# Kernel optimization log

Measured on AMD Instinct MI355X. Metric: run time of the kernel, lower is better.

Reference implementation:

```python
import jax, jax.numpy as jnp
import numpy as np

NUM_HEADS = 16
ROPE_BASE = 10000.0


def _rope_interleaved(x, cos, sin):
    # x: (B, S, H, hd); cos/sin: (1, S, 1, hd//2)
    x1 = x[..., ::2]
    x2 = x[..., 1::2]
    r1 = x1 * cos - x2 * sin
    r2 = x1 * sin + x2 * cos
    return jnp.stack([r1, r2], axis=-1).reshape(x.shape)


def _rope_tables(seq_len, head_dim, dtype):
    dim = head_dim // 2
    freqs = jnp.exp(-jnp.arange(0, dim, dtype=dtype) * jnp.log(jnp.asarray(ROPE_BASE, dtype)) / dim)
    pos = jnp.arange(seq_len, dtype=dtype)
    angles = pos[:, None] * freqs[None, :]  # (S, hd//2)
    return jnp.cos(angles)[None, :, None, :], jnp.sin(angles)[None, :, None, :]


def setup_inputs() -> dict:
    key = jax.random.key(0)
    ks = jax.random.split(key, 9)
    B, S, D = 2, 2048, 2048
    sc = 1.0 / np.sqrt(D)
    return {
        "x": jax.random.normal(ks[0], (B, S, D), jnp.float32),
        "wq": jax.random.normal(ks[1], (D, D), jnp.float32) * sc,
        "bq": jax.random.normal(ks[2], (D,), jnp.float32) * 0.01,
        "wk": jax.random.normal(ks[3], (D, D), jnp.float32) * sc,
        "bk": jax.random.normal(ks[4], (D,), jnp.float32) * 0.01,
        "wv": jax.random.normal(ks[5], (D, D), jnp.float32) * sc,
        "bv": jax.random.normal(ks[6], (D,), jnp.float32) * 0.01,
        "wo": jax.random.normal(ks[7], (D, D), jnp.float32) * sc,
        "bo": jax.random.normal(ks[8], (D,), jnp.float32) * 0.01,
    }


def reference(x, wq, bq, wk, bk, wv, bv, wo, bo):
    B, S, D = x.shape
    H = NUM_HEADS
    hd = D // H
    # QKV projections (eqx.nn.Linear: y = W @ x + b, weight (out, in))
    q = (x @ wq.T + bq).reshape(B, S, H, hd)
    k = (x @ wk.T + bk).reshape(B, S, H, hd)
    v = (x @ wv.T + bv).reshape(B, S, H, hd)
    # RoPE (interleaved / GPT-NeoX style)
    cos, sin = _rope_tables(S, hd, x.dtype)
    q = _rope_interleaved(q, cos, sin)
    k = _rope_interleaved(k, cos, sin)
    # Causal scaled dot-product attention
    scale = 1.0 / np.sqrt(hd)
    scores = jnp.einsum("bqhd,bkhd->bhqk", q, k) * scale
    causal = jnp.tril(jnp.ones((S, S), dtype=bool))
    scores = jnp.where(causal[None, None, :, :], scores, jnp.finfo(scores.dtype).min)
    attn = jax.nn.softmax(scores, axis=-1)
    out = jnp.einsum("bhqk,bkhd->bqhd", attn, v).reshape(B, S, D)
    return out @ wo.T + bo
```

## Files before the change

kernel.cpp:

```cpp
#include <hip/hip_runtime.h>

typedef unsigned short u16;
typedef short bf16x8 __attribute__((ext_vector_type(8)));
typedef float f32x4 __attribute__((ext_vector_type(4)));

#define B_ 2
#define S_ 2048
#define D_ 2048
#define HD_ 128
#define GW 512
#define KB 64
#define VST 72
#define PST 72

__device__ __forceinline__ float bf2f(u16 h) {
  unsigned u = ((unsigned)h) << 16;
  return __builtin_bit_cast(float, u);
}
__device__ __forceinline__ u16 f2bf(float f) {
  unsigned u = __builtin_bit_cast(unsigned, f);
  u += 0x7FFF + ((u >> 16) & 1);
  return (u16)(u >> 16);
}
__device__ __forceinline__ bf16x8 cvt8(const float* p) {
  float4 a = *(const float4*)p;
  float4 b = *(const float4*)(p + 4);
  bf16x8 r;
  r[0] = (short)f2bf(a.x); r[1] = (short)f2bf(a.y);
  r[2] = (short)f2bf(a.z); r[3] = (short)f2bf(a.w);
  r[4] = (short)f2bf(b.x); r[5] = (short)f2bf(b.y);
  r[6] = (short)f2bf(b.z); r[7] = (short)f2bf(b.w);
  return r;
}

__device__ __forceinline__ void gload16(const void* g, void* lds) {
  __builtin_amdgcn_global_load_lds(
      (const __attribute__((address_space(1))) unsigned*)g,
      (__attribute__((address_space(3))) unsigned*)lds, 16, 0, 0);
}

__device__ __forceinline__ f32x4 mfma16(bf16x8 a, bf16x8 b, f32x4 c) {
  return __builtin_amdgcn_mfma_f32_16x16x32_bf16(a, b, c, 0, 0, 0);
}

__global__ void k_cvt_all(const float* __restrict__ x, const float* __restrict__ wq,
                          const float* __restrict__ wk, const float* __restrict__ wv,
                          const float* __restrict__ wo, u16* __restrict__ xb,
                          u16* __restrict__ wqkvb, u16* __restrict__ wob) {
  const int slice = blockIdx.y;
  const int i = blockIdx.x * 256 + threadIdx.x;
  const float* src;
  u16* dst;
  int n8;
  if (slice == 0) { src = x; dst = xb; n8 = 1048576; }
  else if (slice == 1) { src = wq; dst = wqkvb; n8 = 524288; }
  else if (slice == 2) { src = wk; dst = wqkvb + 4194304; n8 = 524288; }
  else if (slice == 3) { src = wv; dst = wqkvb + 8388608; n8 = 524288; }
  else { src = wo; dst = wob; n8 = 524288; }
  if (i < n8) *(bf16x8*)(dst + (size_t)i * 8) = cvt8(src + (size_t)i * 8);
}

template <int AM, int WM, int CM>
__device__ __forceinline__ void gemm_body(const void* Ap, const void* Wp,
                                          const float* __restrict__ bias,
                                          void* Cp, int ldc) {
  constexpr int K = 2048;
  __shared__ u16 As[128 * 32];
  __shared__ u16 Bs[128 * 32];
  const int t = threadIdx.x;
  const int w = t >> 6, l = t & 63, lr = l & 15, lg = l >> 4;
  const int m0 = blockIdx.y * 128, n0 = blockIdx.x * 128;
  const int wr = w >> 1, wc = w & 1;

  f32x4 acc[4][4];
#pragma unroll
  for (int i = 0; i < 4; ++i)
#pragma unroll
    for (int j = 0; j < 4; ++j) acc[i][j] = f32x4{0.f, 0.f, 0.f, 0.f};

  const int rowA0 = t >> 2, ko0 = (t & 3) * 8;
  const int rowA1 = (t + 256) >> 2, ko1 = ((t + 256) & 3) * 8;

  for (int kt = 0; kt < K; kt += 32) {
    if constexpr (AM == 1) {
      const u16* A = (const u16*)Ap;
      gload16(A + (size_t)(m0 + rowA0) * K + kt + ko0, (char*)As + (size_t)w * 1024);
      gload16(A + (size_t)(m0 + rowA1) * K + kt + ko1, (char*)As + (size_t)(w + 4) * 1024);
    } else {
      const float* A = (const float*)Ap;
      *(bf16x8*)((char*)As + (size_t)t * 16) = cvt8(A + (size_t)(m0 + rowA0) * K + kt + ko0);
      *(bf16x8*)((char*)As + (size_t)(t + 256) * 16) = cvt8(A + (size_t)(m0 + rowA1) * K + kt + ko1);
    }
    if constexpr (WM == 1) {
      const u16* W = (const u16*)Wp;
      gload16(W + (size_t)(n0 + rowA0) * K + kt + ko0, (char*)Bs + (size_t)w * 1024);
      gload16(W + (size_t)(n0 + rowA1) * K + kt + ko1, (char*)Bs + (size_t)(w + 4) * 1024);
    } else {
      const float* W = (const float*)Wp;
      *(bf16x8*)((char*)Bs + (size_t)t * 16) = cvt8(W + (size_t)(n0 + rowA0) * K + kt + ko0);
      *(bf16x8*)((char*)Bs + (size_t)(t + 256) * 16) = cvt8(W + (size_t)(n0 + rowA1) * K + kt + ko1);
    }
    __syncthreads();

    bf16x8 af[4], bw[4];
#pragma unroll
    for (int i = 0; i < 4; ++i) {
      af[i] = *(const bf16x8*)(As + (size_t)(wr * 64 + i * 16 + lr) * 32 + lg * 8);
      bw[i] = *(const bf16x8*)(Bs + (size_t)(wc * 64 + i * 16 + lr) * 32 + lg * 8);
    }
#pragma unroll
    for (int i = 0; i < 4; ++i)
#pragma unroll
      for (int j = 0; j < 4; ++j)
        acc[i][j] = mfma16(af[i], bw[j], acc[i][j]);
    __syncthreads();
  }

#pragma unroll
  for (int i = 0; i < 4; ++i) {
#pragma unroll
    for (int j = 0; j < 4; ++j) {
      const int col = n0 + wc * 64 + j * 16 + lr;
      const float bv = bias[col];
      const int row = m0 + wr * 64 + i * 16 + lg * 4;
#pragma unroll
      for (int r = 0; r < 4; ++r) {
        if constexpr (CM == 1)
          ((float*)Cp)[(size_t)(row + r) * ldc + col] = acc[i][j][r] + bv;
        else
          ((u16*)Cp)[(size_t)(row + r) * ldc + col] = f2bf(acc[i][j][r] + bv);
      }
    }
  }
}

__global__ __launch_bounds__(256) void k_gemm_qkv_bb(
    const u16* __restrict__ xb, const u16* __restrict__ wqkvb,
    const float* __restrict__ bq, const float* __restrict__ bk,
    const float* __restrict__ bv, u16* __restrict__ q, u16* __restrict__ k,
    u16* __restrict__ v) {
  const int z = blockIdx.z;
  const u16* W = wqkvb + (size_t)z * D_ * D_;
  const float* bias = z == 0 ? bq : (z == 1 ? bk : bv);
  u16* C = z == 0 ? q : (z == 1 ? k : v);
  gemm_body<1, 1, 0>(xb, W, bias, C, D_);
}

__global__ __launch_bounds__(256) void k_gemm_out_bb(
    const u16* __restrict__ ao, const u16* __restrict__ wob,
    const float* __restrict__ bo, float* __restrict__ out) {
  gemm_body<1, 1, 1>(ao, wob, bo, out, D_);
}

__global__ __launch_bounds__(256) void k_gemm_qkv_xb(
    const u16* __restrict__ xb, const float* __restrict__ wq,
    const float* __restrict__ bq, const float* __restrict__ wk,
    const float* __restrict__ bk, const float* __restrict__ wv,
    const float* __restrict__ bv, u16* __restrict__ q, u16* __restrict__ k,
    u16* __restrict__ v) {
  const int z = blockIdx.z;
  const float* W = z == 0 ? wq : (z == 1 ? wk : wv);
  const float* bias = z == 0 ? bq : (z == 1 ? bk : bv);
  u16* C = z == 0 ? q : (z == 1 ? k : v);
  gemm_body<1, 0, 0>(xb, W, bias, C, D_);
}

__global__ __launch_bounds__(256) void k_gemm_out(const u16* __restrict__ ao,
                                                  const float* __restrict__ wo,
                                                  const float* __restrict__ bo,
                                                  float* __restrict__ out) {
  gemm_body<1, 0, 1>(ao, wo, bo, out, D_);
}

__global__ __launch_bounds__(256) void k_gemm_qkv_g(
    const float* __restrict__ x, const float* __restrict__ wq,
    const float* __restrict__ bq, const float* __restrict__ wk,
    const float* __restrict__ bk, const float* __restrict__ wv,
    const float* __restrict__ bv, u16* __restrict__ qg, u16* __restrict__ kg,
    u16* __restrict__ vg, int g) {
  const int z = blockIdx.z;
  const float* W = (z == 0 ? wq : (z == 1 ? wk : wv)) + (size_t)g * GW * D_;
  const float* bias = (z == 0 ? bq : (z == 1 ? bk : bv)) + g * GW;
  u16* C = z == 0 ? qg : (z == 1 ? kg : vg);
  gemm_body<0, 0, 0>(x, W, bias, C, GW);
}

__device__ __forceinline__ void rope_one(u16* p, float cv, float sv) {
  unsigned u = *(const unsigned*)p;
  float x1 = bf2f((u16)(u & 0xffff)), x2 = bf2f((u16)(u >> 16));
  unsigned r = (unsigned)f2bf(x1 * cv - x2 * sv) |
               ((unsigned)f2bf(x1 * sv + x2 * cv) << 16);
  *(unsigned*)p = r;
}

__global__ void k_rope_full(u16* q, u16* kk) {
  const int idx = blockIdx.x * 256 + threadIdx.x;
  const int i = idx & 63;
  const int hh = (idx >> 6) & 15;
  const int bs = idx >> 10;
  const int s = bs & (S_ - 1);
  const float freq = expf(-(float)i * 0.14391157f);
  float sv, cv;
  sincosf((float)s * freq, &sv, &cv);
  const size_t off = (size_t)bs * D_ + (size_t)hh * HD_ + 2 * i;
  rope_one(q + off, cv, sv);
  rope_one(kk + off, cv, sv);
}

__global__ void k_rope_g(u16* q, u16* kk) {
  const int idx = blockIdx.x * 256 + threadIdx.x;
  const int i = idx & 63;
  const int hh = (idx >> 6) & 3;
  const int bs = idx >> 8;
  const int s = bs & (S_ - 1);
  const float freq = expf(-(float)i * 0.14391157f);
  float sv, cv;
  sincosf((float)s * freq, &sv, &cv);
  const size_t off = (size_t)bs * GW + (size_t)hh * HD_ + 2 * i;
  rope_one(q + off, cv, sv);
  rope_one(kk + off, cv, sv);
}

__device__ __forceinline__ void attn_body(const u16* Q, const u16* Kd,
                                          const u16* V, u16* O,
                                          size_t base_in, size_t base_out,
                                          int ld_in, int ld_out, int q0) {
  const int t = threadIdx.x, w = t >> 6, l = t & 63, lr = l & 15, lg = l >> 4;

  __shared__ u16 Ks[KB * HD_];
  __shared__ u16 Vt[HD_ * VST];
  __shared__ u16 Ps[4][16 * PST];

  bf16x8 qf[4];
  {
    const u16* qp = Q + base_in + (size_t)(q0 + w * 16 + lr) * ld_in;
#pragma unroll
    for (int ds = 0; ds < 4; ++ds)
      qf[ds] = *(const bf16x8*)(qp + ds * 32 + lg * 8);
  }

  f32x4 oacc[8];
#pragma unroll
  for (int f = 0; f < 8; ++f) oacc[f] = f32x4{0.f, 0.f, 0.f, 0.f};
  float mrow = -1e30f, lrow = 0.f;

  const int qrow = q0 + w * 16 + lr;
  const int ntiles = q0 / KB + 1;
  const float sc = 0.08838834764831845f;

  for (int tkv = 0; tkv < ntiles; ++tkv) {
    const int kv0 = tkv * KB;
#pragma unroll
    for (int r = 0; r < 4; ++r) {
      const int c = t + 256 * r;
      const int row = c >> 4, c16 = c & 15;
      const int gc = c16 ^ (row & 7);
      gload16(Kd + base_in + (size_t)(kv0 + row) * ld_in + gc * 8,
              (char*)Ks + (size_t)(w + 4 * r) * 1024);
    }
#pragma unroll
    for (int r = 0; r < 2; ++r) {
      const int c = t + 256 * r;
      const int kk2 = (c & 31) * 2, d0 = (c >> 5) * 8;
      bf16x8 v0 = *(const bf16x8*)(V + base_in + (size_t)(kv0 + kk2) * ld_in + d0);
      bf16x8 v1 = *(const bf16x8*)(V + base_in + (size_t)(kv0 + kk2 + 1) * ld_in + d0);
#pragma unroll
      for (int j = 0; j < 8; ++j) {
        unsigned pk = (unsigned)(unsigned short)v0[j] |
                      ((unsigned)(unsigned short)v1[j] << 16);
        *(unsigned*)&Vt[(size_t)(d0 + j) * VST + kk2] = pk;
      }
    }
    __syncthreads();

    float p[16];
#pragma unroll
    for (int h = 0; h < 4; ++h) {
      f32x4 s = {0.f, 0.f, 0.f, 0.f};
#pragma unroll
      for (int ds = 0; ds < 4; ++ds) {
        const int ch = (ds * 4 + lg) ^ (lr & 7);
        bf16x8 kf = *(const bf16x8*)(Ks + (size_t)(h * 16 + lr) * HD_ + ch * 8);
        s = mfma16(kf, qf[ds], s);
      }
#pragma unroll
      for (int r = 0; r < 4; ++r) p[h * 4 + r] = s[r] * sc;
    }
    if (kv0 + KB - 1 > q0 + w * 16) {
#pragma unroll
      for (int h = 0; h < 4; ++h)
#pragma unroll
        for (int r = 0; r < 4; ++r)
          if (kv0 + h * 16 + lg * 4 + r > qrow) p[h * 4 + r] = -1e30f;
    }
    float pm = p[0];
#pragma unroll
    for (int i = 1; i < 16; ++i) pm = fmaxf(pm, p[i]);
    pm = fmaxf(pm, __shfl_xor(pm, 16, 64));
    pm = fmaxf(pm, __shfl_xor(pm, 32, 64));
    const float mn = fmaxf(mrow, pm);
    const float scl = __expf(mrow - mn);
    mrow = mn;
    float rs = 0.f;
#pragma unroll
    for (int i = 0; i < 16; ++i) {
      p[i] = __expf(p[i] - mn);
      rs += p[i];
    }
    rs += __shfl_xor(rs, 16, 64);
    rs += __shfl_xor(rs, 32, 64);
    lrow = lrow * scl + rs;
    float sj[4];
#pragma unroll
    for (int j = 0; j < 4; ++j) sj[j] = __shfl(scl, lg * 4 + j, 64);
#pragma unroll
    for (int f = 0; f < 8; ++f)
#pragma unroll
      for (int j = 0; j < 4; ++j) oacc[f][j] *= sj[j];
#pragma unroll
    for (int h = 0; h < 4; ++h)
#pragma unroll
      for (int r = 0; r < 4; ++r)
        Ps[w][lr * PST + h * 16 + lg * 4 + r] = f2bf(p[h * 4 + r]);
    bf16x8 pf0 = *(const bf16x8*)&Ps[w][lr * PST + lg * 8];
    bf16x8 pf1 = *(const bf16x8*)&Ps[w][lr * PST + 32 + lg * 8];
#pragma unroll
    for (int f = 0; f < 8; ++f) {
      bf16x8 vf0 = *(const bf16x8*)&Vt[(size_t)(f * 16 + lr) * VST + lg * 8];
      bf16x8 vf1 = *(const bf16x8*)&Vt[(size_t)(f * 16 + lr) * VST + 32 + lg * 8];
      oacc[f] = mfma16(pf0, vf0, oacc[f]);
      oacc[f] = mfma16(pf1, vf1, oacc[f]);
    }
    __syncthreads();
  }

  const float inv = 1.0f / lrow;
  float ij[4];
#pragma unroll
  for (int j = 0; j < 4; ++j) ij[j] = __shfl(inv, lg * 4 + j, 64);
  u16* Op = O + base_out;
#pragma unroll
  for (int f = 0; f < 8; ++f)
#pragma unroll
    for (int j = 0; j < 4; ++j)
      Op[(size_t)(q0 + w * 16 + lg * 4 + j) * ld_out + f * 16 + lr] =
          f2bf(oacc[f][j] * ij[j]);
}

__global__ __launch_bounds__(256) void k_attn_full(const u16* Q, const u16* Kd,
                                                   const u16* V, u16* O) {
  const int lin = blockIdx.y * gridDim.x + blockIdx.x;
  const int work = (lin & 7) * 64 + (lin >> 3);
  const int bh = work >> 4;
  const int pr = work & 15;
  const int b = bh >> 4, h = bh & 15;
  const size_t base = ((size_t)b * S_) * D_ + (size_t)h * HD_;
  attn_body(Q, Kd, V, O, base, base, D_, D_, 64 * (31 - pr));
  attn_body(Q, Kd, V, O, base, base, D_, D_, 64 * pr);
}

__global__ __launch_bounds__(256) void k_attn_g(const u16* __restrict__ Q,
                                                const u16* __restrict__ Kd,
                                                const u16* __restrict__ V,
                                                u16* __restrict__ O, int g) {
  const int by = blockIdx.y;
  const int b = by >> 2, hh = by & 3;
  const size_t base_in = ((size_t)b * S_) * GW + (size_t)hh * HD_;
  const size_t base_out = ((size_t)b * S_) * D_ + (size_t)(g * 4 + hh) * HD_;
  attn_body(Q, Kd, V, O, base_in, base_out, GW, D_, blockIdx.x * 64);
}

extern "C" void kernel_launch(void* const* d_in, const int* in_sizes, int n_in,
                              void* d_out, int out_size, void* d_ws,
                              size_t ws_size, hipStream_t stream) {
  (void)in_sizes; (void)n_in; (void)out_size;
  const float* x = (const float*)d_in[0];
  const float* wq = (const float*)d_in[1];
  const float* bq = (const float*)d_in[2];
  const float* wk = (const float*)d_in[3];
  const float* bk = (const float*)d_in[4];
  const float* wv = (const float*)d_in[5];
  const float* bv = (const float*)d_in[6];
  const float* wo = (const float*)d_in[7];
  const float* bo = (const float*)d_in[8];
  float* out = (float*)d_out;

  const size_t XB = (size_t)B_ * S_ * D_ * 2;
  const size_t WB3 = 3 * (size_t)D_ * D_ * 2;
  const size_t WB1 = (size_t)D_ * D_ * 2;
  char* ws = (char*)d_ws;
  char* ob = (char*)d_out;

  u16 *xb, *q, *k, *v, *wqkvb = nullptr, *wob = nullptr;
  int tier;
  if (ws_size >= 4 * XB + WB3 + WB1) {
    xb = (u16*)ws; q = (u16*)(ws + XB); k = (u16*)(ws + 2 * XB);
    v = (u16*)(ws + 3 * XB);
    wqkvb = (u16*)(ws + 4 * XB); wob = (u16*)(ws + 4 * XB + WB3);
    tier = 1;
  } else if (ws_size >= 3 * XB + WB3 + WB1) {
    xb = (u16*)ob;
    q = (u16*)ws; k = (u16*)(ws + XB); v = (u16*)(ws + 2 * XB);
    wqkvb = (u16*)(ws + 3 * XB); wob = (u16*)(ws + 3 * XB + WB3);
    tier = 1;
  } else if (ws_size >= 2 * XB + WB3 + WB1) {
    xb = (u16*)ob; v = (u16*)(ob + XB);
    q = (u16*)ws; k = (u16*)(ws + XB);
    wqkvb = (u16*)(ws + 2 * XB); wob = (u16*)(ws + 2 * XB + WB3);
    tier = 1;
  } else if (ws_size >= 2 * XB) {
    xb = (u16*)ob; v = (u16*)(ob + XB);
    q = (u16*)ws; k = (u16*)(ws + XB);
    tier = 2;
  } else {
    tier = 3;
  }

  if (tier == 1) {
    dim3 gc(4096, 5);
    k_cvt_all<<<gc, 256, 0, stream>>>(x, wq, wk, wv, wo, xb, wqkvb, wob);
    dim3 g1(16, 32, 3);
    k_gemm_qkv_bb<<<g1, 256, 0, stream>>>(xb, wqkvb, bq, bk, bv, q, k, v);
    k_rope_full<<<16384, 256, 0, stream>>>(q, k);
    dim3 g2(16, 32);
    k_attn_full<<<g2, 256, 0, stream>>>(q, k, v, q);
    dim3 g3(16, 32);
    k_gemm_out_bb<<<g3, 256, 0, stream>>>(q, wob, bo, out);
  } else if (tier == 2) {
    dim3 gc(4096, 1);
    k_cvt_all<<<gc, 256, 0, stream>>>(x, wq, wk, wv, wo, xb, xb, xb);
    dim3 g1(16, 32, 3);
    k_gemm_qkv_xb<<<g1, 256, 0, stream>>>(xb, wq, bq, wk, bk, wv, bv, q, k, v);
    k_rope_full<<<16384, 256, 0, stream>>>(q, k);
    dim3 g2(16, 32);
    k_attn_full<<<g2, 256, 0, stream>>>(q, k, v, q);
    dim3 g3(16, 32);
    k_gemm_out<<<g3, 256, 0, stream>>>(q, wo, bo, out);
  } else {
    u16* qg = (u16*)ob;
    u16* kg = qg + (size_t)(B_ * S_) * GW;
    u16* vg = kg + (size_t)(B_ * S_) * GW;
    u16* ao = (u16*)ws;
    for (int g = 0; g < 4; ++g) {
      dim3 g1(4, 32, 3);
      k_gemm_qkv_g<<<g1, 256, 0, stream>>>(x, wq, bq, wk, bk, wv, bv, qg, kg, vg, g);
      k_rope_g<<<4096, 256, 0, stream>>>(qg, kg);
      dim3 g2(32, 8);
      k_attn_g<<<g2, 256, 0, stream>>>(qg, kg, vg, ao, g);
    }
    dim3 g3(16, 32);
    k_gemm_out<<<g3, 256, 0, stream>>>(ao, wo, bo, out);
  }
}
```

Before: 293.0 us.

## Fuse RoPE into QKV GEMM epilogue and double-buffer K/V in attention

Precomputes a cos/sin table inside the conversion kernel and applies RoPE in the QKV GEMM epilogue, using a lane shuffle to pair interleaved columns. This removes the separate RoPE pass over Q and K. The attention loop now double-buffers K (async LDS loads) and V (register prefetch), uses explicit waitcnt/s_barrier and raises wave priority around the MFMA sections, so the next tile's loads overlap compute. Doubling the K/V shared memory may lower occupancy, and workspace tiers are reshuffled to hold the table.

```diff
diff --git a/kernel.cpp b/kernel.cpp
--- a/kernel.cpp
+++ b/kernel.cpp
@@ -46,9 +46,20 @@
 __global__ void k_cvt_all(const float* __restrict__ x, const float* __restrict__ wq,
                           const float* __restrict__ wk, const float* __restrict__ wv,
                           const float* __restrict__ wo, u16* __restrict__ xb,
-                          u16* __restrict__ wqkvb, u16* __restrict__ wob) {
+                          u16* __restrict__ wqkvb, u16* wob, float2* tab) {
   const int slice = blockIdx.y;
   const int i = blockIdx.x * 256 + threadIdx.x;
+  if (slice == 5) {
+    if (tab != nullptr && i < 131072) {
+      const int s = i >> 6, ip = i & 63;
+      const float freq = expf(-(float)ip * 0.14391157f);
+      float sv, cv;
+      sincosf((float)s * freq, &sv, &cv);
+      tab[i] = make_float2(cv, sv);
+    }
+    return;
+  }
+  if (slice == 4 && wob == nullptr) return;
   const float* src;
   u16* dst;
   int n8;
@@ -63,7 +74,8 @@
 template <int AM, int WM, int CM>
 __device__ __forceinline__ void gemm_body(const void* Ap, const void* Wp,
                                           const float* __restrict__ bias,
-                                          void* Cp, int ldc) {
+                                          void* Cp, int ldc,
+                                          const float2* __restrict__ tab) {
   constexpr int K = 2048;
   __shared__ u16 As[128 * 32];
   __shared__ u16 Bs[128 * 32];
@@ -123,12 +135,25 @@
       const int col = n0 + wc * 64 + j * 16 + lr;
       const float bv = bias[col];
       const int row = m0 + wr * 64 + i * 16 + lg * 4;
-#pragma unroll
-      for (int r = 0; r < 4; ++r) {
-        if constexpr (CM == 1)
-          ((float*)Cp)[(size_t)(row + r) * ldc + col] = acc[i][j][r] + bv;
-        else
-          ((u16*)Cp)[(size_t)(row + r) * ldc + col] = f2bf(acc[i][j][r] + bv);
+      if (CM == 0 && tab != nullptr) {
+        const int ip = (col & 127) >> 1;
+        const int odd = col & 1;
+#pragma unroll
+        for (int r = 0; r < 4; ++r) {
+          const float v = acc[i][j][r] + bv;
+          const float p = __shfl_xor(v, 1, 64);
+          const float2 cs = tab[((row + r) & (S_ - 1)) * 64 + ip];
+          const float o = odd ? (p * cs.y + v * cs.x) : (v * cs.x - p * cs.y);
+          ((u16*)Cp)[(size_t)(row + r) * ldc + col] = f2bf(o);
+        }
+      } else {
+#pragma unroll
+        for (int r = 0; r < 4; ++r) {
+          if constexpr (CM == 1)
+            ((float*)Cp)[(size_t)(row + r) * ldc + col] = acc[i][j][r] + bv;
+          else
+            ((u16*)Cp)[(size_t)(row + r) * ldc + col] = f2bf(acc[i][j][r] + bv);
+        }
       }
     }
   }
@@ -138,18 +163,18 @@
     const u16* __restrict__ xb, const u16* __restrict__ wqkvb,
     const float* __restrict__ bq, const float* __restrict__ bk,
     const float* __restrict__ bv, u16* __restrict__ q, u16* __restrict__ k,
-    u16* __restrict__ v) {
+    u16* __restrict__ v, const float2* __restrict__ tab) {
   const int z = blockIdx.z;
   const u16* W = wqkvb + (size_t)z * D_ * D_;
   const float* bias = z == 0 ? bq : (z == 1 ? bk : bv);
   u16* C = z == 0 ? q : (z == 1 ? k : v);
-  gemm_body<1, 1, 0>(xb, W, bias, C, D_);
+  gemm_body<1, 1, 0>(xb, W, bias, C, D_, z == 2 ? nullptr : tab);
 }
 
 __global__ __launch_bounds__(256) void k_gemm_out_bb(
     const u16* __restrict__ ao, const u16* __restrict__ wob,
     const float* __restrict__ bo, float* __restrict__ out) {
-  gemm_body<1, 1, 1>(ao, wob, bo, out, D_);
+  gemm_body<1, 1, 1>(ao, wob, bo, out, D_, nullptr);
 }
 
 __global__ __launch_bounds__(256) void k_gemm_qkv_xb(
@@ -162,14 +187,14 @@
   const float* W = z == 0 ? wq : (z == 1 ? wk : wv);
   const float* bias = z == 0 ? bq : (z == 1 ? bk : bv);
   u16* C = z == 0 ? q : (z == 1 ? k : v);
-  gemm_body<1, 0, 0>(xb, W, bias, C, D_);
+  gemm_body<1, 0, 0>(xb, W, bias, C, D_, nullptr);
 }
 
 __global__ __launch_bounds__(256) void k_gemm_out(const u16* __restrict__ ao,
                                                   const float* __restrict__ wo,
                                                   const float* __restrict__ bo,
                                                   float* __restrict__ out) {
-  gemm_body<1, 0, 1>(ao, wo, bo, out, D_);
+  gemm_body<1, 0, 1>(ao, wo, bo, out, D_, nullptr);
 }
 
 __global__ __launch_bounds__(256) void k_gemm_qkv_g(
@@ -182,7 +207,7 @@
   const float* W = (z == 0 ? wq : (z == 1 ? wk : wv)) + (size_t)g * GW * D_;
   const float* bias = (z == 0 ? bq : (z == 1 ? bk : bv)) + g * GW;
   u16* C = z == 0 ? qg : (z == 1 ? kg : vg);
-  gemm_body<0, 0, 0>(x, W, bias, C, GW);
+  gemm_body<0, 0, 0>(x, W, bias, C, GW, nullptr);
 }
 
 __device__ __forceinline__ void rope_one(u16* p, float cv, float sv) {
@@ -227,8 +252,8 @@
                                           int ld_in, int ld_out, int q0) {
   const int t = threadIdx.x, w = t >> 6, l = t & 63, lr = l & 15, lg = l >> 4;
 
-  __shared__ u16 Ks[KB * HD_];
-  __shared__ u16 Vt[HD_ * VST];
+  __shared__ u16 Ks[2][KB * HD_];
+  __shared__ u16 Vt[2][HD_ * VST];
   __shared__ u16 Ps[4][16 * PST];
 
   bf16x8 qf[4];
@@ -245,47 +270,90 @@
   float mrow = -1e30f, lrow = 0.f;
 
   const int qrow = q0 + w * 16 + lr;
-  const int ntiles = q0 / KB + 1;
+  const int nt = q0 / KB + 1;
   const float sc = 0.08838834764831845f;
 
-  for (int tkv = 0; tkv < ntiles; ++tkv) {
-    const int kv0 = tkv * KB;
-#pragma unroll
-    for (int r = 0; r < 4; ++r) {
-      const int c = t + 256 * r;
-      const int row = c >> 4, c16 = c & 15;
-      const int gc = c16 ^ (row & 7);
-      gload16(Kd + base_in + (size_t)(kv0 + row) * ld_in + gc * 8,
-              (char*)Ks + (size_t)(w + 4 * r) * 1024);
-    }
-#pragma unroll
-    for (int r = 0; r < 2; ++r) {
-      const int c = t + 256 * r;
-      const int kk2 = (c & 31) * 2, d0 = (c >> 5) * 8;
-      bf16x8 v0 = *(const bf16x8*)(V + base_in + (size_t)(kv0 + kk2) * ld_in + d0);
-      bf16x8 v1 = *(const bf16x8*)(V + base_in + (size_t)(kv0 + kk2 + 1) * ld_in + d0);
+  const int kRow = t >> 4, kC16 = t & 15;
+  (void)kRow; (void)kC16;
+  const int c1 = t + 256;
+  const int kk20 = (t & 31) * 2, d00 = (t >> 5) * 8;
+  const int kk21 = (c1 & 31) * 2, d01 = (c1 >> 5) * 8;
+
+  bf16x8 vc[4];
+
+#pragma unroll
+  for (int r = 0; r < 4; ++r) {
+    const int c = t + 256 * r;
+    const int row = c >> 4, c16 = c & 15;
+    const int gc = c16 ^ (row & 7);
+    gload16(Kd + base_in + (size_t)row * ld_in + gc * 8,
+            (char*)Ks[0] + (size_t)(w + 4 * r) * 1024);
+  }
+  vc[0] = *(const bf16x8*)(V + base_in + (size_t)kk20 * ld_in + d00);
+  vc[1] = *(const bf16x8*)(V + base_in + (size_t)(kk20 + 1) * ld_in + d00);
+  vc[2] = *(const bf16x8*)(V + base_in + (size_t)kk21 * ld_in + d01);
+  vc[3] = *(const bf16x8*)(V + base_in + (size_t)(kk21 + 1) * ld_in + d01);
+
+  for (int tt = 0; tt < nt; ++tt) {
+    const int cur = tt & 1;
+    const int kv0 = tt * KB;
+    const bool more = (tt + 1 < nt);
+
+    if (more) {
+      const int kvn = kv0 + KB;
+#pragma unroll
+      for (int r = 0; r < 4; ++r) {
+        const int c = t + 256 * r;
+        const int row = c >> 4, c16 = c & 15;
+        const int gc = c16 ^ (row & 7);
+        gload16(Kd + base_in + (size_t)(kvn + row) * ld_in + gc * 8,
+                (char*)Ks[cur ^ 1] + (size_t)(w + 4 * r) * 1024);
+      }
+      asm volatile("s_waitcnt vmcnt(4)" ::: "memory");
+    } else {
+      asm volatile("s_waitcnt vmcnt(0)" ::: "memory");
+    }
+    __builtin_amdgcn_sched_barrier(0);
+
+    {
+      u16* vt = Vt[cur];
 #pragma unroll
       for (int j = 0; j < 8; ++j) {
-        unsigned pk = (unsigned)(unsigned short)v0[j] |
-                      ((unsigned)(unsigned short)v1[j] << 16);
-        *(unsigned*)&Vt[(size_t)(d0 + j) * VST + kk2] = pk;
+        unsigned p0 = (unsigned)(unsigned short)vc[0][j] |
+                      ((unsigned)(unsigned short)vc[1][j] << 16);
+        *(unsigned*)&vt[(size_t)(d00 + j) * VST + kk20] = p0;
+        unsigned p1 = (unsigned)(unsigned short)vc[2][j] |
+                      ((unsigned)(unsigned short)vc[3][j] << 16);
+        *(unsigned*)&vt[(size_t)(d01 + j) * VST + kk21] = p1;
       }
     }
-    __syncthreads();
+    if (more) {
+      const int kvn = kv0 + KB;
+      vc[0] = *(const bf16x8*)(V + base_in + (size_t)(kvn + kk20) * ld_in + d00);
+      vc[1] = *(const bf16x8*)(V + base_in + (size_t)(kvn + kk20 + 1) * ld_in + d00);
+      vc[2] = *(const bf16x8*)(V + base_in + (size_t)(kvn + kk21) * ld_in + d01);
+      vc[3] = *(const bf16x8*)(V + base_in + (size_t)(kvn + kk21 + 1) * ld_in + d01);
+    }
+    asm volatile("s_waitcnt lgkmcnt(0)" ::: "memory");
+    __builtin_amdgcn_sched_barrier(0);
+    __builtin_amdgcn_s_barrier();
+    __builtin_amdgcn_sched_barrier(0);
 
     float p[16];
+    __builtin_amdgcn_s_setprio(1);
 #pragma unroll
     for (int h = 0; h < 4; ++h) {
       f32x4 s = {0.f, 0.f, 0.f, 0.f};
 #pragma unroll
       for (int ds = 0; ds < 4; ++ds) {
         const int ch = (ds * 4 + lg) ^ (lr & 7);
-        bf16x8 kf = *(const bf16x8*)(Ks + (size_t)(h * 16 + lr) * HD_ + ch * 8);
+        bf16x8 kf = *(const bf16x8*)(Ks[cur] + (size_t)(h * 16 + lr) * HD_ + ch * 8);
         s = mfma16(kf, qf[ds], s);
       }
 #pragma unroll
       for (int r = 0; r < 4; ++r) p[h * 4 + r] = s[r] * sc;
     }
+    __builtin_amdgcn_s_setprio(0);
     if (kv0 + KB - 1 > q0 + w * 16) {
 #pragma unroll
       for (int h = 0; h < 4; ++h)
@@ -324,14 +392,18 @@
         Ps[w][lr * PST + h * 16 + lg * 4 + r] = f2bf(p[h * 4 + r]);
     bf16x8 pf0 = *(const bf16x8*)&Ps[w][lr * PST + lg * 8];
     bf16x8 pf1 = *(const bf16x8*)&Ps[w][lr * PST + 32 + lg * 8];
+    __builtin_amdgcn_s_setprio(1);
 #pragma unroll
     for (int f = 0; f < 8; ++f) {
-      bf16x8 vf0 = *(const bf16x8*)&Vt[(size_t)(f * 16 + lr) * VST + lg * 8];
-      bf16x8 vf1 = *(const bf16x8*)&Vt[(size_t)(f * 16 + lr) * VST + 32 + lg * 8];
+      bf16x8 vf0 = *(const bf16x8*)&Vt[cur][(size_t)(f * 16 + lr) * VST + lg * 8];
+      bf16x8 vf1 = *(const bf16x8*)&Vt[cur][(size_t)(f * 16 + lr) * VST + 32 + lg * 8];
       oacc[f] = mfma16(pf0, vf0, oacc[f]);
       oacc[f] = mfma16(pf1, vf1, oacc[f]);
     }
-    __syncthreads();
+    __builtin_amdgcn_s_setprio(0);
+    __builtin_amdgcn_sched_barrier(0);
+    __builtin_amdgcn_s_barrier();
+    __builtin_amdgcn_sched_barrier(0);
   }
 
   const float inv = 1.0f / lrow;
@@ -388,47 +460,54 @@
   const size_t XB = (size_t)B_ * S_ * D_ * 2;
   const size_t WB3 = 3 * (size_t)D_ * D_ * 2;
   const size_t WB1 = (size_t)D_ * D_ * 2;
+  const size_t TB = (size_t)S_ * 64 * 8;
   char* ws = (char*)d_ws;
   char* ob = (char*)d_out;
 
   u16 *xb, *q, *k, *v, *wqkvb = nullptr, *wob = nullptr;
+  float2* tab = nullptr;
   int tier;
-  if (ws_size >= 4 * XB + WB3 + WB1) {
+  if (ws_size >= 4 * XB + WB3 + WB1 + TB) {
     xb = (u16*)ws; q = (u16*)(ws + XB); k = (u16*)(ws + 2 * XB);
     v = (u16*)(ws + 3 * XB);
     wqkvb = (u16*)(ws + 4 * XB); wob = (u16*)(ws + 4 * XB + WB3);
+    tab = (float2*)(ws + 4 * XB + WB3 + WB1);
     tier = 1;
-  } else if (ws_size >= 3 * XB + WB3 + WB1) {
+  } else if (ws_size >= 3 * XB + WB3 + WB1 + TB) {
     xb = (u16*)ob;
     q = (u16*)ws; k = (u16*)(ws + XB); v = (u16*)(ws + 2 * XB);
     wqkvb = (u16*)(ws + 3 * XB); wob = (u16*)(ws + 3 * XB + WB3);
+    tab = (float2*)(ws + 3 * XB + WB3 + WB1);
     tier = 1;
-  } else if (ws_size >= 2 * XB + WB3 + WB1) {
+  } else if (ws_size >= 2 * XB + WB3 + TB) {
     xb = (u16*)ob; v = (u16*)(ob + XB);
     q = (u16*)ws; k = (u16*)(ws + XB);
-    wqkvb = (u16*)(ws + 2 * XB); wob = (u16*)(ws + 2 * XB + WB3);
-    tier = 1;
+    wqkvb = (u16*)(ws + 2 * XB);
+    tab = (float2*)(ws + 2 * XB + WB3);
+    tier = 2;
   } else if (ws_size >= 2 * XB) {
     xb = (u16*)ob; v = (u16*)(ob + XB);
     q = (u16*)ws; k = (u16*)(ws + XB);
-    tier = 2;
+    tier = 3;
   } else {
-    tier = 3;
-  }
-
-  if (tier == 1) {
-    dim3 gc(4096, 5);
-    k_cvt_all<<<gc, 256, 0, stream>>>(x, wq, wk, wv, wo, xb, wqkvb, wob);
+    tier = 4;
+  }
+
+  if (tier == 1 || tier == 2) {
+    dim3 gc(4096, 6);
+    k_cvt_all<<<gc, 256, 0, stream>>>(x, wq, wk, wv, wo, xb, wqkvb, wob, tab);
     dim3 g1(16, 32, 3);
-    k_gemm_qkv_bb<<<g1, 256, 0, stream>>>(xb, wqkvb, bq, bk, bv, q, k, v);
-    k_rope_full<<<16384, 256, 0, stream>>>(q, k);
+    k_gemm_qkv_bb<<<g1, 256, 0, stream>>>(xb, wqkvb, bq, bk, bv, q, k, v, tab);
     dim3 g2(16, 32);
     k_attn_full<<<g2, 256, 0, stream>>>(q, k, v, q);
     dim3 g3(16, 32);
-    k_gemm_out_bb<<<g3, 256, 0, stream>>>(q, wob, bo, out);
-  } else if (tier == 2) {
+    if (tier == 1)
+      k_gemm_out_bb<<<g3, 256, 0, stream>>>(q, wob, bo, out);
+    else
+      k_gemm_out<<<g3, 256, 0, stream>>>(q, wo, bo, out);
+  } else if (tier == 3) {
     dim3 gc(4096, 1);
-    k_cvt_all<<<gc, 256, 0, stream>>>(x, wq, wk, wv, wo, xb, xb, xb);
+    k_cvt_all<<<gc, 256, 0, stream>>>(x, wq, wk, wv, wo, xb, xb, nullptr, nullptr);
     dim3 g1(16, 32, 3);
     k_gemm_qkv_xb<<<g1, 256, 0, stream>>>(xb, wq, bq, wk, bk, wv, bv, q, k, v);
     k_rope_full<<<16384, 256, 0, stream>>>(q, k);
```

New measurement: 280.0 us. 4.4% less time.
